# Kernel tuning notes

Hardware: AMD Instinct MI355X
Metric: run time of the kernel (lower is better)

Reference implementation:

```python
import jax, jax.numpy as jnp
import numpy as np

EMB_DIM = 1024
NUM_HEADS = 16
HEAD_DIM = EMB_DIM // NUM_HEADS  # 64
B, S = 2, 2048


def setup_inputs() -> dict:
    key = jax.random.key(0)
    ks = jax.random.split(key, 9)
    scale = 1.0 / np.sqrt(EMB_DIM)
    return {
        "query": jax.random.normal(ks[0], (B, S, EMB_DIM), dtype=jnp.float32),
        "Wq": jax.random.normal(ks[1], (EMB_DIM, EMB_DIM), dtype=jnp.float32) * scale,
        "bq": jax.random.normal(ks[2], (EMB_DIM,), dtype=jnp.float32) * 0.01,
        "Wk": jax.random.normal(ks[3], (EMB_DIM, EMB_DIM), dtype=jnp.float32) * scale,
        "bk": jax.random.normal(ks[4], (EMB_DIM,), dtype=jnp.float32) * 0.01,
        "Wv": jax.random.normal(ks[5], (EMB_DIM, EMB_DIM), dtype=jnp.float32) * scale,
        "bv": jax.random.normal(ks[6], (EMB_DIM,), dtype=jnp.float32) * 0.01,
        "Wo": jax.random.normal(ks[7], (EMB_DIM, EMB_DIM), dtype=jnp.float32) * scale,
        "bo": jax.random.normal(ks[8], (EMB_DIM,), dtype=jnp.float32) * 0.01,
    }


def reference(query, Wq, bq, Wk, bk, Wv, bv, Wo, bo):
    # Self-attention path (key_value=None, mask=None in the original forward).
    b, s, _ = query.shape
    # torch nn.Linear: y = x @ W.T + b
    def proj(x, W, bias):
        y = jnp.einsum('bse,fe->bsf', x, W) + bias
        # [B,S,E] -> [B,H,S,D]
        return y.reshape(b, s, NUM_HEADS, HEAD_DIM).transpose(0, 2, 1, 3)

    q = proj(query, Wq, bq)
    k = proj(query, Wk, bk)
    v = proj(query, Wv, bv)

    scores = jnp.einsum('bhqd,bhkd->bhqk', q, k) / np.sqrt(HEAD_DIM).astype(np.float32)
    attn = jax.nn.softmax(scores, axis=-1)  # [B,H,S,S]
    out = jnp.einsum('bhqk,bhkd->bhqd', attn, v)
    out = out.transpose(0, 2, 1, 3).reshape(b, s, EMB_DIM)
    return jnp.einsum('bse,fe->bsf', out, Wo) + bo
```

## Files before the change

kernel.cpp:

```cpp
#include <hip/hip_runtime.h>
#include <hip/hip_bf16.h>

using bf16x4 = __attribute__((ext_vector_type(4))) short;
using short8 = __attribute__((ext_vector_type(8))) short;
using f32x4  = __attribute__((ext_vector_type(4))) float;
using f32x16 = __attribute__((ext_vector_type(16))) float;
using u32x2  = __attribute__((ext_vector_type(2))) unsigned;

__device__ __forceinline__ short f2bf(float f) {
  unsigned u = __builtin_bit_cast(unsigned, f);
  u = (u + 0x7fffu + ((u >> 16) & 1u)) >> 16;
  return (short)u;
}
__device__ __forceinline__ unsigned pk2(float a, float b) {
  __hip_bfloat162 h = __float22bfloat162_rn(make_float2(a, b));
  unsigned u; __builtin_memcpy(&u, &h, 4);
  return u;
}
__device__ __forceinline__ void gload16(const short* g, short* l) {
  __builtin_amdgcn_global_load_lds(
      (const __attribute__((address_space(1))) unsigned int*)g,
      (__attribute__((address_space(3))) unsigned int*)l, 16, 0, 0);
}
__device__ __forceinline__ void pl32swap(unsigned &a, unsigned &b) {
  asm("v_permlane32_swap_b32 %0, %1" : "+v"(a), "+v"(b));
}

constexpr int E  = 1024;
constexpr int SL = 2048;
constexpr int NB = 2;
constexpr int NH = 16;
constexpr int M  = NB * SL;

__global__ __launch_bounds__(256) void convert_kernel(
    const float* __restrict__ X,  const float* __restrict__ Wq,
    const float* __restrict__ Wk, const float* __restrict__ Wv,
    const float* __restrict__ Wo, short* __restrict__ out)
{
  const size_t i8 = ((size_t)blockIdx.x * 256 + threadIdx.x) * 8;
  const float* src;
  if (i8 < (size_t)(4u << 20)) {
    src = X + i8;
  } else {
    size_t r = i8 - (size_t)(4u << 20);
    int wi = (int)(r >> 20);
    size_t off = r & ((1u << 20) - 1);
    src = (wi == 0 ? Wq : wi == 1 ? Wk : wi == 2 ? Wv : Wo) + off;
  }
  f32x4 a = *(const f32x4*)src;
  f32x4 b = *(const f32x4*)(src + 4);
  short hb[8];
#pragma unroll
  for (int e = 0; e < 4; ++e) { hb[e] = f2bf(a[e]); hb[4 + e] = f2bf(b[e]); }
  *(short8*)(out + i8) = *(short8*)hb;
}

template <int TM, int TN, bool OUTF32, bool FUSEV>
__global__ __launch_bounds__(256) void gemm_kernel(
    const short* __restrict__ A0, const short* __restrict__ A1, const short* __restrict__ A2,
    const short* __restrict__ W0, const short* __restrict__ W1, const short* __restrict__ W2,
    const float* __restrict__ b0, const float* __restrict__ b1, const float* __restrict__ b2,
    void* __restrict__ Y0, void* __restrict__ Y1, void* __restrict__ Y2,
    float s0, float s1, float s2, int ld0, int ld1, int ld2)
{
  constexpr int BK = 32;
  constexpr int RA = TM / 64;
  constexpr int RB = TN / 64;
  constexpr int WM = TM / 2, WN = TN / 2;
  constexpr int NI = WM / 16, NJ = WN / 16;
  __shared__ alignas(16) short As[2][TM * BK];
  __shared__ alignas(16) short Bs[2][TN * BK];
  const int t = threadIdx.x;
  const int l = t & 63;
  const int w = t >> 6;
  const int c = l & 15;
  const int g = l >> 4;
  const int z = blockIdx.z;
  const short* Ap = (z == 0) ? A0 : (z == 1) ? A1 : A2;
  const short* Wp = (z == 0) ? W0 : (z == 1) ? W1 : W2;
  const float* bp = (z == 0) ? b0 : (z == 1) ? b1 : b2;
  void* Yp        = (z == 0) ? Y0 : (z == 1) ? Y1 : Y2;
  const float sc  = (z == 0) ? s0 : (z == 1) ? s1 : s2;
  const int ldY   = (z == 0) ? ld0 : (z == 1) ? ld1 : ld2;
  const bool vtr  = FUSEV && (z == 2);
  const int m0 = (vtr ? blockIdx.y : blockIdx.x) * TM;
  const int n0 = (vtr ? blockIdx.x : blockIdx.y) * TN;

  const short* gA[RA]; int oA[RA];
  const short* gB[RB]; int oB[RB];
#pragma unroll
  for (int r = 0; r < RA; ++r) {
    const int cc = r * 256 + t;
    gA[r] = Ap + (size_t)(m0 + (cc >> 2)) * E + (cc & 3) * 8;
    oA[r] = (r * 256 + (t & ~63)) * 8;
  }
#pragma unroll
  for (int r = 0; r < RB; ++r) {
    const int cc = r * 256 + t;
    gB[r] = Wp + (size_t)(n0 + (cc >> 2)) * E + (cc & 3) * 8;
    oB[r] = (r * 256 + (t & ~63)) * 8;
  }

#pragma unroll
  for (int r = 0; r < RA; ++r) gload16(gA[r], &As[0][oA[r]]);
#pragma unroll
  for (int r = 0; r < RB; ++r) gload16(gB[r], &Bs[0][oB[r]]);

  const int wm = (w >> 1) * WM;
  const int wn = (w & 1) * WN;
  f32x4 acc[NI][NJ] = {};
  int cur = 0;

  for (int k0 = 0; k0 < E; k0 += BK) {
    __syncthreads();
    if (k0 + BK < E) {
#pragma unroll
      for (int r = 0; r < RA; ++r) gload16(gA[r] + k0 + BK, &As[cur ^ 1][oA[r]]);
#pragma unroll
      for (int r = 0; r < RB; ++r) gload16(gB[r] + k0 + BK, &Bs[cur ^ 1][oB[r]]);
    }
    short8 ah[NI], bfr[NJ];
#pragma unroll
    for (int i = 0; i < NI; ++i)
      ah[i] = *(const short8*)&As[cur][(wm + i * 16 + c) * BK + g * 8];
#pragma unroll
    for (int j = 0; j < NJ; ++j)
      bfr[j] = *(const short8*)&Bs[cur][(wn + j * 16 + c) * BK + g * 8];
#pragma unroll
    for (int i = 0; i < NI; ++i)
#pragma unroll
      for (int j = 0; j < NJ; ++j)
        acc[i][j] = __builtin_amdgcn_mfma_f32_16x16x32_bf16(ah[i], bfr[j], acc[i][j], 0, 0, 0);
    cur ^= 1;
  }

#pragma unroll
  for (int j = 0; j < NJ; ++j) {
    const int col = n0 + wn + j * 16 + c;
    const float bcol = vtr ? 0.f : bp[col];
#pragma unroll
    for (int i = 0; i < NI; ++i) {
      const int rowb = m0 + wm + i * 16 + g * 4;
#pragma unroll
      for (int r = 0; r < 4; ++r) {
        const int row = rowb + r;
        const float bias = vtr ? bp[row] : bcol;
        const float v = (acc[i][j][r] + bias) * sc;
        if (OUTF32) ((float*)Yp)[(size_t)row * ldY + col] = v;
        else        ((short*)Yp)[(size_t)row * ldY + col] = f2bf(v);
      }
    }
  }
}

__global__ __launch_bounds__(256, 2) void flash_kernel(
    const short* __restrict__ Qm, const short* __restrict__ Km,
    const short* __restrict__ VTm, short* __restrict__ Oh)
{
  __shared__ alignas(16) short Ks[2][64][64];
  __shared__ alignas(16) short Vt[2][64][64];
  const int t = threadIdx.x;
  const int l = t & 63;
  const int w = t >> 6;
  const int c = l & 31;
  const int hi = l >> 5;
  const int q0 = blockIdx.x * 128;
  const int bh = (int)blockIdx.y;
  const int bat = bh >> 4;
  const int h = bh & 15;
  const size_t baseK = (size_t)bat * SL * E + h * 64;
  const size_t baseV = (size_t)(h * 64) * M + (size_t)bat * SL;

  short8 qf[4];
  {
    const short* qp = Qm + baseK + (size_t)(q0 + w * 32 + c) * E + hi * 8;
#pragma unroll
    for (int tt = 0; tt < 4; ++tt) qf[tt] = *(const short8*)(qp + tt * 16);
  }

  const int sr = t >> 3, sg = t & 7;
  const int swz = (sg ^ (sr & 7)) * 8;
  const short* gK0 = Km + baseK + (size_t)sr * E + sg * 8;
  const short* gK1 = gK0 + (size_t)32 * E;
  const short* gV0 = VTm + baseV + (size_t)sr * M + sg * 8;
  const short* gV1 = gV0 + (size_t)32 * M;
  const int wo0 = sr * 64 + swz;
  const int wo1 = (sr + 32) * 64 + swz;

  short8 k0r, k1r, v0r, v1r;
  k0r = *(const short8*)gK0; k1r = *(const short8*)gK1;
  v0r = *(const short8*)gV0; v1r = *(const short8*)gV1;
  *(short8*)(&Ks[0][0][0] + wo0) = k0r; *(short8*)(&Ks[0][0][0] + wo1) = k1r;
  *(short8*)(&Vt[0][0][0] + wo0) = v0r; *(short8*)(&Vt[0][0][0] + wo1) = v1r;
  k0r = *(const short8*)(gK0 + (size_t)64 * E);
  k1r = *(const short8*)(gK1 + (size_t)64 * E);
  v0r = *(const short8*)(gV0 + 64);
  v1r = *(const short8*)(gV1 + 64);

  f32x16 oa0 = {}, oa1 = {};
  f32x4 lacc = {0.f, 0.f, 0.f, 0.f};
  __syncthreads();

  constexpr int NTT = SL / 64;
  const int sx = c & 7;
  for (int kt = 0; kt < NTT; ++kt) {
    const int cur = kt & 1;
    if (kt + 1 < NTT) {
      short* Kn = &Ks[cur ^ 1][0][0];
      short* Vn = &Vt[cur ^ 1][0][0];
      *(short8*)(Kn + wo0) = k0r; *(short8*)(Kn + wo1) = k1r;
      *(short8*)(Vn + wo0) = v0r; *(short8*)(Vn + wo1) = v1r;
      if (kt + 2 < NTT) {
        const size_t ko = (size_t)(kt + 2) * 64 * E;
        const int vo = (kt + 2) * 64;
        k0r = *(const short8*)(gK0 + ko); k1r = *(const short8*)(gK1 + ko);
        v0r = *(const short8*)(gV0 + vo); v1r = *(const short8*)(gV1 + vo);
      }
    }
    const short* Kc0 = &Ks[cur][c][0];
    const short* Kc1 = &Ks[cur][32 + c][0];
    const short* Vc0 = &Vt[cur][c][0];
    const short* Vc1 = &Vt[cur][32 + c][0];

    f32x16 st0 = {}, st1 = {};
#pragma unroll
    for (int tt = 0; tt < 4; ++tt) {
      const int off = ((tt * 2 + hi) ^ sx) * 8;
      short8 kf0 = *(const short8*)(Kc0 + off);
      short8 kf1 = *(const short8*)(Kc1 + off);
      st0 = __builtin_amdgcn_mfma_f32_32x32x16_bf16(kf0, qf[tt], st0, 0, 0, 0);
      st1 = __builtin_amdgcn_mfma_f32_32x32x16_bf16(kf1, qf[tt], st1, 0, 0, 0);
    }

    float p0[16], p1[16];
#pragma unroll
    for (int i = 0; i < 16; ++i) p0[i] = __builtin_amdgcn_exp2f(st0[i]);
#pragma unroll
    for (int i = 0; i < 16; ++i) p1[i] = __builtin_amdgcn_exp2f(st1[i]);
#pragma unroll
    for (int i = 0; i < 16; ++i) lacc[i & 3] += p0[i] + p1[i];

    unsigned W0[4][2], W1[4][2];
#pragma unroll
    for (int b8 = 0; b8 < 4; ++b8) {
      W0[b8][0] = pk2(p0[4 * b8 + 0], p0[4 * b8 + 1]);
      W0[b8][1] = pk2(p0[4 * b8 + 2], p0[4 * b8 + 3]);
      W1[b8][0] = pk2(p1[4 * b8 + 0], p1[4 * b8 + 1]);
      W1[b8][1] = pk2(p1[4 * b8 + 2], p1[4 * b8 + 3]);
    }

#pragma unroll
    for (int tt = 0; tt < 4; ++tt) {
      unsigned a0, a1, b0, b1;
      if (tt == 0)      { a0 = W0[0][0]; a1 = W0[0][1]; b0 = W0[1][0]; b1 = W0[1][1]; }
      else if (tt == 1) { a0 = W0[2][0]; a1 = W0[2][1]; b0 = W0[3][0]; b1 = W0[3][1]; }
      else if (tt == 2) { a0 = W1[0][0]; a1 = W1[0][1]; b0 = W1[1][0]; b1 = W1[1][1]; }
      else              { a0 = W1[2][0]; a1 = W1[2][1]; b0 = W1[3][0]; b1 = W1[3][1]; }
      pl32swap(a0, b0);
      pl32swap(a1, b1);
      union { unsigned u[4]; short8 s8; } pf;
      pf.u[0] = a0; pf.u[1] = a1; pf.u[2] = b0; pf.u[3] = b1;
      const int off = ((tt * 2 + hi) ^ sx) * 8;
      short8 vf0 = *(const short8*)(Vc0 + off);
      short8 vf1 = *(const short8*)(Vc1 + off);
      oa0 = __builtin_amdgcn_mfma_f32_32x32x16_bf16(vf0, pf.s8, oa0, 0, 0, 0);
      oa1 = __builtin_amdgcn_mfma_f32_32x32x16_bf16(vf1, pf.s8, oa1, 0, 0, 0);
    }
    __syncthreads();
  }

  float s = lacc[0] + lacc[1] + lacc[2] + lacc[3];
  s += __shfl_xor(s, 32);
  const float inv = 1.0f / s;
  const int q = q0 + w * 32 + c;
  short* op = Oh + ((size_t)bat * SL + q) * E + h * 64 + hi * 4;
#pragma unroll
  for (int b8 = 0; b8 < 4; ++b8) {
    u32x2 t0 = {pk2(oa0[4 * b8 + 0] * inv, oa0[4 * b8 + 1] * inv),
                pk2(oa0[4 * b8 + 2] * inv, oa0[4 * b8 + 3] * inv)};
    *(u32x2*)(op + b8 * 8) = t0;
    u32x2 t1 = {pk2(oa1[4 * b8 + 0] * inv, oa1[4 * b8 + 1] * inv),
                pk2(oa1[4 * b8 + 2] * inv, oa1[4 * b8 + 3] * inv)};
    *(u32x2*)(op + 32 + b8 * 8) = t1;
  }
}

extern "C" void kernel_launch(void* const* d_in, const int* in_sizes, int n_in,
                              void* d_out, int out_size, void* d_ws, size_t ws_size,
                              hipStream_t stream)
{
  const float* X  = (const float*)d_in[0];
  const float* Wq = (const float*)d_in[1];
  const float* bq = (const float*)d_in[2];
  const float* Wk = (const float*)d_in[3];
  const float* bk = (const float*)d_in[4];
  const float* Wv = (const float*)d_in[5];
  const float* bv = (const float*)d_in[6];
  const float* Wo = (const float*)d_in[7];
  const float* bo = (const float*)d_in[8];
  float* out = (float*)d_out;

  const size_t szX = (size_t)M * E;
  const size_t szW = (size_t)E * E;
  short* Xb  = (short*)d_ws;
  short* Wqb = Xb + szX;
  short* Wkb = Wqb + szW;
  short* Wvb = Wkb + szW;
  short* Wob = Wvb + szW;
  short* Qw  = Wob + szW;
  short* Kw  = Qw + szX;
  short* VTw = Kw + szX;

  convert_kernel<<<4096, 256, 0, stream>>>(X, Wq, Wk, Wv, Wo, Xb);

  const float kLog2eOver8 = 0.18033688011112042f;
  dim3 g1(M / 128, E / 128, 3);
  gemm_kernel<128, 128, false, true><<<g1, 256, 0, stream>>>(
      Xb, Xb, Wvb,
      Wqb, Wkb, Xb,
      bq, bk, bv,
      (void*)Qw, (void*)Kw, (void*)VTw,
      kLog2eOver8, 1.0f, 1.0f, E, E, M);

  dim3 g2(SL / 128, NB * NH);
  flash_kernel<<<g2, 256, 0, stream>>>(Qw, Kw, VTw, Qw );

  dim3 g3(M / 128, E / 64, 1);
  gemm_kernel<128, 64, true, false><<<g3, 256, 0, stream>>>(
      Qw, Qw, Qw,
      Wob, Wob, Wob,
      bo, bo, bo,
      (void*)out, (void*)out, (void*)out,
      1.0f, 1.0f, 1.0f, E, E, E);
}
```

Baseline: 206.6 us.

## Swap GEMM operand roles so epilogue stores are vectorized along rows

The GEMM now computes the transposed product (weights as A, activations as B) for Q, K and the output projection. Each lane's four accumulator values are then contiguous in memory and go out as packed bf16x4 or float4 stores instead of scalar stores. Row biases are preloaded once per thread. The output projection also moves from a 128x64 tile to a 128x128 tile, which halves its block count but may lower occupancy and load balance.

Result: faster. 198.1 us (-4.1%).

```diff
diff --git a/kernel.cpp b/kernel.cpp
--- a/kernel.cpp
+++ b/kernel.cpp
@@ -55,15 +55,16 @@
   *(short8*)(out + i8) = *(short8*)hb;
 }
 
-template <int TM, int TN, bool OUTF32, bool FUSEV>
+template <bool OUTF32, bool PROJ>
 __global__ __launch_bounds__(256) void gemm_kernel(
     const short* __restrict__ A0, const short* __restrict__ A1, const short* __restrict__ A2,
-    const short* __restrict__ W0, const short* __restrict__ W1, const short* __restrict__ W2,
+    const short* __restrict__ B0, const short* __restrict__ B1, const short* __restrict__ B2,
     const float* __restrict__ b0, const float* __restrict__ b1, const float* __restrict__ b2,
     void* __restrict__ Y0, void* __restrict__ Y1, void* __restrict__ Y2,
     float s0, float s1, float s2, int ld0, int ld1, int ld2)
 {
   constexpr int BK = 32;
+  constexpr int TM = 128, TN = 128;
   constexpr int RA = TM / 64;
   constexpr int RB = TN / 64;
   constexpr int WM = TM / 2, WN = TN / 2;
@@ -77,14 +78,14 @@
   const int g = l >> 4;
   const int z = blockIdx.z;
   const short* Ap = (z == 0) ? A0 : (z == 1) ? A1 : A2;
-  const short* Wp = (z == 0) ? W0 : (z == 1) ? W1 : W2;
+  const short* Bp = (z == 0) ? B0 : (z == 1) ? B1 : B2;
   const float* bp = (z == 0) ? b0 : (z == 1) ? b1 : b2;
   void* Yp        = (z == 0) ? Y0 : (z == 1) ? Y1 : Y2;
   const float sc  = (z == 0) ? s0 : (z == 1) ? s1 : s2;
   const int ldY   = (z == 0) ? ld0 : (z == 1) ? ld1 : ld2;
-  const bool vtr  = FUSEV && (z == 2);
-  const int m0 = (vtr ? blockIdx.y : blockIdx.x) * TM;
-  const int n0 = (vtr ? blockIdx.x : blockIdx.y) * TN;
+  const bool swp  = PROJ ? (z != 2) : true;
+  const int m0 = (swp ? blockIdx.y : blockIdx.x) * TM;
+  const int n0 = (swp ? blockIdx.x : blockIdx.y) * TN;
 
   const short* gA[RA]; int oA[RA];
   const short* gB[RB]; int oB[RB];
@@ -97,7 +98,7 @@
 #pragma unroll
   for (int r = 0; r < RB; ++r) {
     const int cc = r * 256 + t;
-    gB[r] = Wp + (size_t)(n0 + (cc >> 2)) * E + (cc & 3) * 8;
+    gB[r] = Bp + (size_t)(n0 + (cc >> 2)) * E + (cc & 3) * 8;
     oB[r] = (r * 256 + (t & ~63)) * 8;
   }
 
@@ -134,20 +135,31 @@
     cur ^= 1;
   }
 
+  float bm[NI][4];
+  if (swp) {
+#pragma unroll
+    for (int i = 0; i < NI; ++i)
+#pragma unroll
+      for (int r = 0; r < 4; ++r)
+        bm[i][r] = bp[m0 + wm + i * 16 + g * 4 + r];
+  }
 #pragma unroll
   for (int j = 0; j < NJ; ++j) {
     const int col = n0 + wn + j * 16 + c;
-    const float bcol = vtr ? 0.f : bp[col];
+    const float bj = swp ? 0.f : bp[col];
 #pragma unroll
     for (int i = 0; i < NI; ++i) {
-      const int rowb = m0 + wm + i * 16 + g * 4;
-#pragma unroll
-      for (int r = 0; r < 4; ++r) {
-        const int row = rowb + r;
-        const float bias = vtr ? bp[row] : bcol;
-        const float v = (acc[i][j][r] + bias) * sc;
-        if (OUTF32) ((float*)Yp)[(size_t)row * ldY + col] = v;
-        else        ((short*)Yp)[(size_t)row * ldY + col] = f2bf(v);
+      const int row = m0 + wm + i * 16 + g * 4;
+      float v[4];
+#pragma unroll
+      for (int r = 0; r < 4; ++r)
+        v[r] = (acc[i][j][r] + (swp ? bm[i][r] : bj)) * sc;
+      if (OUTF32) {
+        f32x4 o = {v[0], v[1], v[2], v[3]};
+        *(f32x4*)((float*)Yp + (size_t)col * ldY + row) = o;
+      } else {
+        u32x2 o = {pk2(v[0], v[1]), pk2(v[2], v[3])};
+        *(u32x2*)((short*)Yp + (size_t)col * ldY + row) = o;
       }
     }
   }
@@ -315,9 +327,9 @@
 
   const float kLog2eOver8 = 0.18033688011112042f;
   dim3 g1(M / 128, E / 128, 3);
-  gemm_kernel<128, 128, false, true><<<g1, 256, 0, stream>>>(
+  gemm_kernel<false, true><<<g1, 256, 0, stream>>>(
+      Wqb, Wkb, Xb,
       Xb, Xb, Wvb,
-      Wqb, Wkb, Xb,
       bq, bk, bv,
       (void*)Qw, (void*)Kw, (void*)VTw,
       kLog2eOver8, 1.0f, 1.0f, E, E, M);
@@ -325,10 +337,10 @@
   dim3 g2(SL / 128, NB * NH);
   flash_kernel<<<g2, 256, 0, stream>>>(Qw, Kw, VTw, Qw );
 
-  dim3 g3(M / 128, E / 64, 1);
-  gemm_kernel<128, 64, true, false><<<g3, 256, 0, stream>>>(
+  dim3 g3(M / 128, E / 128, 1);
+  gemm_kernel<true, false><<<g3, 256, 0, stream>>>(
+      Wob, Wob, Wob,
       Qw, Qw, Qw,
-      Wob, Wob, Wob,
       bo, bo, bo,
       (void*)out, (void*)out, (void*)out,
       1.0f, 1.0f, 1.0f, E, E, E);
```
